# Kernel tuning notes

Hardware: AMD Instinct MI355X
Metric: run time of the kernel (lower is better)

Reference implementation:

```python
import jax, jax.numpy as jnp
import numpy as np

KH, KW = 3, 3
STRIDE, PAD = 2, 1
NEG_SLOPE = 0.2
EPS = 1e-5


def conv2d(x, w, stride, pad):
    return jax.lax.conv_general_dilated(
        x, w, window_strides=(stride, stride),
        padding=[(pad, pad), (pad, pad)],
        dimension_numbers=('NCHW', 'OIHW', 'NCHW'))


def deform_conv2d(x, offsets, w_def):
    # x: [B,C,H,W]; offsets: [B,2*K,Ho,Wo] (per-kernel-tap (dy,dx) pairs);
    # w_def: [Cout,Cin,KH,KW]. Matches torchvision DeformConv2d (v1, no mask).
    B, C, H, W = x.shape
    Ho, Wo = offsets.shape[2], offsets.shape[3]
    K = KH * KW
    off = offsets.reshape(B, K, 2, Ho, Wo)
    dy, dx = off[:, :, 0], off[:, :, 1]            # [B,K,Ho,Wo]

    ky = jnp.arange(KH).repeat(KW).astype(x.dtype)   # [K]
    kx = jnp.tile(jnp.arange(KW), KH).astype(x.dtype)
    base_y = (jnp.arange(Ho) * STRIDE - PAD).astype(x.dtype)  # [Ho]
    base_x = (jnp.arange(Wo) * STRIDE - PAD).astype(x.dtype)

    # sampling positions [B,K,Ho,Wo]
    py = base_y[None, None, :, None] + ky[None, :, None, None] + dy
    px = base_x[None, None, None, :] + kx[None, :, None, None] + dx

    y0f = jnp.floor(py); x0f = jnp.floor(px)
    wy1 = py - y0f; wy0 = 1.0 - wy1
    wx1 = px - x0f; wx0 = 1.0 - wx1
    y0 = y0f.astype(jnp.int32); x0 = x0f.astype(jnp.int32)
    y1 = y0 + 1; x1 = x0 + 1

    xt = jnp.transpose(x, (0, 2, 3, 1))  # [B,H,W,C] for channel-last gather
    bidx = jnp.arange(B)[:, None, None, None]

    def corner(yi, xi):
        valid = ((yi >= 0) & (yi < H) & (xi >= 0) & (xi < W)).astype(x.dtype)
        yc = jnp.clip(yi, 0, H - 1); xc = jnp.clip(xi, 0, W - 1)
        v = xt[bidx, yc, xc]                         # [B,K,Ho,Wo,C]
        return v * valid[..., None]

    sampled = (corner(y0, x0) * (wy0 * wx0)[..., None]
               + corner(y0, x1) * (wy0 * wx1)[..., None]
               + corner(y1, x0) * (wy1 * wx0)[..., None]
               + corner(y1, x1) * (wy1 * wx1)[..., None])  # [B,K,Ho,Wo,C]

    wk = w_def.reshape(w_def.shape[0], w_def.shape[1], K)   # [Cout,Cin,K]
    return jnp.einsum('bkhwc,ock->bohw', sampled, wk)


def leaky_relu(x):
    return jnp.where(x >= 0, x, NEG_SLOPE * x)


def instance_norm(x):
    mean = jnp.mean(x, axis=(2, 3), keepdims=True)
    var = jnp.var(x, axis=(2, 3), keepdims=True)
    return (x - mean) * jax.lax.rsqrt(var + EPS)


def setup_inputs() -> dict:
    key = jax.random.key(0)
    k1, k2, k3, k4 = jax.random.split(key, 4)
    B, Cin, H, W = 8, 256, 128, 128
    Cout = 256
    x = jax.random.normal(k1, (B, Cin, H, W), dtype=jnp.float32)
    # conv_offset weight: predicts 2*K offset channels
    w_off = jax.random.normal(k2, (2 * KH * KW, Cin, KH, KW), dtype=jnp.float32) * 0.01
    w_def = jax.random.normal(k3, (Cout, Cin, KH, KW), dtype=jnp.float32) * 0.02
    w_1x1 = jax.random.normal(k4, (Cout, Cout, 1, 1), dtype=jnp.float32) * 0.02
    return {"x": x, "w_off": w_off, "w_def": w_def, "w_1x1": w_1x1}


def reference(x, w_off, w_def, w_1x1):
    offsets = conv2d(x, w_off, STRIDE, PAD)          # [B,18,Ho,Wo]
    y = deform_conv2d(x, offsets, w_def)             # [B,Cout,Ho,Wo]
    y = leaky_relu(y)
    y = conv2d(y, w_1x1, 1, 0)
    y = instance_norm(y)
    return leaky_relu(y)
```

## Files before the change

kernel.cpp:

```cpp
#include <hip/hip_runtime.h>

#define B_   8
#define CIN  256
#define H_   128
#define W_   128
#define HO   64
#define WO   64
#define CO_  256
#define NEG  0.2f

typedef __attribute__((ext_vector_type(8))) _Float16 h16x8;
typedef __attribute__((ext_vector_type(4))) float f32x4;
typedef unsigned short u16;

#define OFF_OFS   0
#define WDEF_OFS  589824
#define W1_OFS    884736
#define WBOFF_OFS 917504
#define Y1_OFS    954368
#define XBF_OFS   5148672
#define TAP_OFS   21925888
#define WS_NEED_TAP ((21925888ull + 1179648ull) * 4ull)

__device__ __forceinline__ float lrelu(float v) { return v >= 0.f ? v : NEG * v; }

__device__ __forceinline__ u16 f2h(float f) {
    _Float16 h = (_Float16)f;
    return *(u16*)&h;
}

__device__ __forceinline__ void gld16(const void* g, void* l) {
    __builtin_amdgcn_global_load_lds((const __attribute__((address_space(1))) unsigned*)g,
                                     (__attribute__((address_space(3))) unsigned*)l, 16, 0, 0);
}

__global__ __launch_bounds__(256) void prep(
    const float* __restrict__ wdef, const float* __restrict__ w1,
    const float* __restrict__ woff,
    u16* __restrict__ wdefh, u16* __restrict__ w1h, u16* __restrict__ wboff)
{
    int i = blockIdx.x * 256 + threadIdx.x;
    if (i < 9 * 256 * 256) {
        int c  = i & 255;
        int co = (i >> 8) & 255;
        int k  = i >> 16;
        wdefh[i] = f2h(wdef[((size_t)co * 256 + c) * 9 + k]);
    }
    if (i < 65536) w1h[i] = f2h(w1[i]);
    if (i < 73728) {
        int j  = i & 7;
        int s  = (i >> 3) & 7;
        int co = (i >> 6) & 31;
        int ch = (i >> 11) & 3;
        int k  = i >> 13;
        int c  = ch * 64 + ((s ^ ((co >> 1) & 7)) << 3) + j;
        wboff[i] = (co < 18) ? f2h(woff[((size_t)co * 256 + c) * 9 + k]) : (u16)0;
    }
}

__global__ __launch_bounds__(256) void nchw2nhwc(
    const float* __restrict__ x, u16* __restrict__ xh)
{
    __shared__ float tile[64][128];
    int bid = blockIdx.x;
    int g = bid & 3;
    int y = (bid >> 2) & 127;
    int b = bid >> 9;
    int t = threadIdx.x;

    const float* src = x + ((size_t)(b * 256 + g * 64) * 128 + y) * 128;
#pragma unroll
    for (int p = 0; p < 8; ++p) {
        int i = p * 256 + t;
        int cc = i >> 5, x4 = (i & 31) * 4;
        *(float4*)&tile[cc][x4] = *(const float4*)(src + (size_t)cc * 16384 + x4);
    }
    __syncthreads();

    int xpos = t >> 1, h = t & 1;
    u16 buf[32];
#pragma unroll
    for (int j = 0; j < 32; ++j) buf[j] = f2h(tile[h * 32 + j][xpos]);
    u16* dst = xh + (((size_t)b * 128 + y) * 128 + xpos) * 256 + g * 64 + h * 32;
#pragma unroll
    for (int q = 0; q < 4; ++q)
        *(int4*)(dst + q * 8) = *(int4*)(buf + q * 8);
}

__global__ __launch_bounds__(256) void offconv_mfma(
    const u16* __restrict__ xh, const u16* __restrict__ wboff,
    float* __restrict__ off)
{
    __shared__ __align__(16) char smem[57728];
    u16* xrowU = (u16*)smem;
    u16* bU    = (u16*)(smem + 49536);

    int blk = blockIdx.x;
    blk = (blk & 7) * 64 + (blk >> 3);
    int b = blk >> 6, ho = blk & 63;
    int t = threadIdx.x;
    int lane = t & 63, w = t >> 6;
    int r = lane & 15, kg = lane >> 4;

    const u16* xB = xh + (size_t)b * (128 * 128 * 256);

    f32x4 acc[2];
    acc[0] = f32x4{0.f, 0.f, 0.f, 0.f};
    acc[1] = f32x4{0.f, 0.f, 0.f, 0.f};

    if (t < 24) {
        int ry = t >> 3, s = t & 7;
        *(int4*)(smem + (ry * 129 * 8 + s) * 16) = int4{0, 0, 0, 0};
    }

    for (int ch = 0; ch < 4; ++ch) {
        __syncthreads();
        for (int ry = 0; ry < 3; ++ry) {
            int y = 2 * ho - 1 + ry;
            int rowbase = (ry * 129 + 1) * 128;
            if ((unsigned)y < 128u) {
#pragma unroll
                for (int p = 0; p < 4; ++p) {
                    int u = p * 256 + t;
                    int xpi = u >> 3, s = u & 7;
                    int c8 = s ^ (((xpi + 1) >> 1) & 7);
                    gld16(xB + ((size_t)(y * 128 + xpi)) * 256 + ch * 64 + c8 * 8,
                          smem + rowbase + p * 4096 + w * 1024);
                }
            } else if (ch == 0) {
#pragma unroll
                for (int p = 0; p < 4; ++p)
                    *(int4*)(smem + rowbase + (p * 256 + t) * 16) = int4{0, 0, 0, 0};
            }
        }
        gld16(wboff + (size_t)(0 * 4 + ch) * 2048 + t * 8,
              smem + 49536 + w * 1024);
        __syncthreads();

        for (int k = 0; k < 9; ++k) {
            int buf = k & 1;
            if (k < 8)
                gld16(wboff + (size_t)((k + 1) * 4 + ch) * 2048 + t * 8,
                      smem + 49536 + (buf ^ 1) * 4096 + w * 1024);
            int ky = k / 3, kx = k - 3 * ky;
            int pixA = w * 16 + r;
            int xp = 2 * pixA + kx;
            int abase = (ky * 129 + xp) * 64;
            int swA = (xp >> 1) & 7;
#pragma unroll
            for (int ksub = 0; ksub < 2; ++ksub) {
                int lc = ksub * 4 + kg;
                h16x8 a = *(h16x8*)(xrowU + abase + ((lc ^ swA) << 3));
#pragma unroll
                for (int n = 0; n < 2; ++n) {
                    int co = n * 16 + r;
                    h16x8 bb = *(h16x8*)(bU + buf * 2048 + co * 64 +
                                         ((lc ^ ((co >> 1) & 7)) << 3));
                    acc[n] = __builtin_amdgcn_mfma_f32_16x16x32_f16(a, bb, acc[n], 0, 0, 0);
                }
            }
            __syncthreads();
        }
    }

#pragma unroll
    for (int n = 0; n < 2; ++n) {
        int co = n * 16 + r;
        if (co < 18) {
#pragma unroll
            for (int j = 0; j < 4; ++j) {
                int wo = w * 16 + kg * 4 + j;
                off[(((size_t)b * 18 + co) * 64 + ho) * 64 + wo] = acc[n][j];
            }
        }
    }
}

__global__ __launch_bounds__(256) void tapgen(
    const float* __restrict__ off, int4* __restrict__ tap)
{
    int bid = blockIdx.x;
    int b = bid >> 6, ho = bid & 63;
    for (int i = threadIdx.x; i < 576; i += 256) {
        int pix = i / 9, k = i - 9 * (i / 9);
        int ky = k / 3, kx = k - 3 * ky;
        float dy = off[(((size_t)b * 18 + 2 * k    ) * 64 + ho) * 64 + pix];
        float dx = off[(((size_t)b * 18 + 2 * k + 1) * 64 + ho) * 64 + pix];
        float py = (float)(ho * 2 - 1 + ky) + dy;
        float px = (float)(pix * 2 - 1 + kx) + dx;
        float y0f = floorf(py), x0f = floorf(px);
        int y0 = (int)y0f, x0i = (int)x0f;
        float wy1 = py - y0f, wx1 = px - x0f;
        float wy0 = 1.f - wy1, wx0 = 1.f - wx1;
        int y1i = y0 + 1, x1i = x0i + 1;
        bool vy0 = (unsigned)y0  < 128u;
        bool vy1 = (unsigned)y1i < 128u;
        bool vx0 = (unsigned)x0i < 128u;
        bool vx1 = (unsigned)x1i < 128u;
        int yc0 = min(max(y0, 0), 127), yc1 = min(max(y1i, 0), 127);
        int xc0 = min(max(x0i, 0), 127), xc1 = min(max(x1i, 0), 127);
        int4 e;
        e.x = (yc0 * 128 + xc0) * 512 | (xc1 - xc0) | ((yc1 - yc0) << 1);
        e.y = (int)((unsigned)f2h((vy0 && vx0) ? wy0 * wx0 : 0.f) |
                    ((unsigned)f2h((vy0 && vx1) ? wy0 * wx1 : 0.f) << 16));
        e.z = (int)((unsigned)f2h((vy1 && vx0) ? wy1 * wx0 : 0.f) |
                    ((unsigned)f2h((vy1 && vx1) ? wy1 * wx1 : 0.f) << 16));
        e.w = 0;
        tap[(size_t)bid * 576 + i] = e;
    }
}

__global__ __launch_bounds__(512, 4) void deform_tap(
    const u16* __restrict__ xh, const int4* __restrict__ tap,
    const u16* __restrict__ wdefh, u16* __restrict__ y1p)
{
    extern __shared__ __align__(16) char smem[];

    int blk = blockIdx.x;
    blk = (blk & 7) * 64 + (blk >> 3);
    int b = blk >> 6, ho = blk & 63;
    int t = threadIdx.x;
    int lane = t & 63, w = t >> 6;
    int r = lane & 15, kg = lane >> 4;
    int pixS = w * 8 + (lane >> 3);
    int cs   = lane & 7;

    f32x4 acc[4][2];
    f32x4 zz = {0.f, 0.f, 0.f, 0.f};
#pragma unroll
    for (int m = 0; m < 4; ++m)
#pragma unroll
        for (int n = 0; n < 2; ++n) acc[m][n] = zz;

    const int4* tapB = tap + (size_t)(b * 64 + ho) * 576 + pixS * 9;
    const char* xb2  = (const char*)(xh + (size_t)b * (128 * 128 * 256)) + cs * 16;

    int sbw = pixS * 128 + ((cs ^ (pixS & 7)) << 4);

    auto stage = [&](int k, int ch, int dbuf) {
        const u16* wk = wdefh + ((size_t)k << 16);
#pragma unroll
        for (int p2 = 0; p2 < 4; ++p2) {
            int i = p2 * 512 + t;
            int co = i >> 3, s = i & 7;
            gld16(wk + (size_t)co * 256 + ch * 64 + ((s ^ (co & 7)) << 3),
                  smem + dbuf * 32768 + p2 * 8192 + w * 1024);
        }
    };

    {
        stage(0, 0, 0);
        int4 e = tapB[0];
        int o00 = e.x & 0x7FFFFE00;
        int dxo = (e.x & 1) << 9;
        int dyo = (e.x & 2) << 15;
        h16x8 c00 = *(const h16x8*)(xb2 + o00);
        h16x8 c01 = *(const h16x8*)(xb2 + o00 + dxo);
        h16x8 c10 = *(const h16x8*)(xb2 + o00 + dyo);
        h16x8 c11 = *(const h16x8*)(xb2 + o00 + dyo + dxo);
        union U { int u; _Float16 h[2]; };
        U u01, u23;
        u01.u = e.y; u23.u = e.z;
        h16x8 v = c00 * u01.h[0] + c01 * u01.h[1] + c10 * u23.h[0] + c11 * u23.h[1];
        *(h16x8*)(smem + 65536 + sbw) = v;
    }
    __syncthreads();

    for (int p = 0; p < 36; ++p) {
        int cur = p & 1;
        bool nx = p < 35;
        int4 e;
        h16x8 c00, c01, c10, c11;
        if (nx) {
            int pn = p + 1;
            int chn = pn / 9, kn = pn - 9 * chn;
            e = tapB[kn];
            int o00 = e.x & 0x7FFFFE00;
            int dxo = (e.x & 1) << 9;
            int dyo = (e.x & 2) << 15;
            const char* base = xb2 + chn * 128;
            c00 = *(const h16x8*)(base + o00);
            c01 = *(const h16x8*)(base + o00 + dxo);
            c10 = *(const h16x8*)(base + o00 + dyo);
            c11 = *(const h16x8*)(base + o00 + dyo + dxo);
            stage(kn, chn, cur ^ 1);
        }
        {
            u16* wb = (u16*)(smem + cur * 32768);
            u16* sb = (u16*)(smem + 65536 + cur * 8192);
            h16x8 af[4], bfr[2];
            __builtin_amdgcn_s_setprio(1);
#pragma unroll
            for (int ksub = 0; ksub < 2; ++ksub) {
                int so = ((ksub * 4 + kg) ^ (r & 7)) << 3;
#pragma unroll
                for (int m = 0; m < 4; ++m)
                    af[m] = *(h16x8*)(sb + (m * 16 + r) * 64 + so);
#pragma unroll
                for (int n = 0; n < 2; ++n)
                    bfr[n] = *(h16x8*)(wb + (w * 32 + n * 16 + r) * 64 + so);
#pragma unroll
                for (int m = 0; m < 4; ++m)
#pragma unroll
                    for (int n = 0; n < 2; ++n)
                        acc[m][n] = __builtin_amdgcn_mfma_f32_16x16x32_f16(af[m], bfr[n], acc[m][n], 0, 0, 0);
            }
            __builtin_amdgcn_s_setprio(0);
        }
        if (nx) {
            union U { int u; _Float16 h[2]; };
            U u01, u23;
            u01.u = e.y; u23.u = e.z;
            h16x8 v = c00 * u01.h[0] + c01 * u01.h[1] + c10 * u23.h[0] + c11 * u23.h[1];
            *(h16x8*)(smem + 65536 + (cur ^ 1) * 8192 + sbw) = v;
        }
        __syncthreads();
    }

    u16* outT = (u16*)smem;
    int rg = lane >> 4;
#pragma unroll
    for (int m = 0; m < 4; ++m)
#pragma unroll
        for (int n = 0; n < 2; ++n) {
            int co = w * 32 + n * 16 + r;
#pragma unroll
            for (int j = 0; j < 4; ++j) {
                int prow = m * 16 + rg * 4 + j;
                outT[prow * 256 + co] = f2h(lrelu(acc[m][n][j]));
            }
        }
    __syncthreads();
    u16* dst = y1p + (size_t)(b * 64 + ho) * 16384;
#pragma unroll
    for (int p = 0; p < 4; ++p)
        *(int4*)((char*)dst + p * 8192 + t * 16) = *(int4*)(smem + p * 8192 + t * 16);
}

__global__ __launch_bounds__(512, 4) void deform_inline(
    const u16* __restrict__ xh, const float* __restrict__ off,
    const u16* __restrict__ wdefh, u16* __restrict__ y1p)
{
    extern __shared__ __align__(16) char smem[];

    int blk = blockIdx.x;
    blk = (blk & 7) * 64 + (blk >> 3);
    int b = blk >> 6, ho = blk & 63;
    int t = threadIdx.x;
    int lane = t & 63, w = t >> 6;
    int r = lane & 15, kg = lane >> 4;
    int pixS = w * 8 + (lane >> 3);
    int cs   = lane & 7;

    f32x4 acc[4][2];
    f32x4 zz = {0.f, 0.f, 0.f, 0.f};
#pragma unroll
    for (int m = 0; m < 4; ++m)
#pragma unroll
        for (int n = 0; n < 2; ++n) acc[m][n] = zz;

    const u16* xB = xh + (size_t)b * (128 * 128 * 256);

    int o00, o01, o10, o11;
    float f00, f01, f10, f11;

    auto coords = [&](int k) {
        int ky = k / 3, kx = k - 3 * ky;
        float dy = off[(((size_t)b * 18 + 2 * k    ) * 64 + ho) * 64 + pixS];
        float dx = off[(((size_t)b * 18 + 2 * k + 1) * 64 + ho) * 64 + pixS];
        float py = (float)(ho * 2 - 1 + ky) + dy;
        float px = (float)(pixS * 2 - 1 + kx) + dx;
        float y0f = floorf(py), x0f = floorf(px);
        int y0 = (int)y0f, x0i = (int)x0f;
        float wy1 = py - y0f, wx1 = px - x0f;
        float wy0 = 1.f - wy1, wx0 = 1.f - wx1;
        int y1i = y0 + 1, x1i = x0i + 1;
        bool vy0 = (unsigned)y0  < 128u;
        bool vy1 = (unsigned)y1i < 128u;
        bool vx0 = (unsigned)x0i < 128u;
        bool vx1 = (unsigned)x1i < 128u;
        int yc0 = min(max(y0, 0), 127), yc1 = min(max(y1i, 0), 127);
        int xc0 = min(max(x0i, 0), 127), xc1 = min(max(x1i, 0), 127);
        o00 = yc0 * 128 + xc0;  o01 = yc0 * 128 + xc1;
        o10 = yc1 * 128 + xc0;  o11 = yc1 * 128 + xc1;
        f00 = (vy0 && vx0) ? wy0 * wx0 : 0.f;
        f01 = (vy0 && vx1) ? wy0 * wx1 : 0.f;
        f10 = (vy1 && vx0) ? wy1 * wx0 : 0.f;
        f11 = (vy1 && vx1) ? wy1 * wx1 : 0.f;
    };

    auto stage = [&](int k, int ch, int dbuf) {
        const u16* wk = wdefh + ((size_t)k << 16);
#pragma unroll
        for (int p2 = 0; p2 < 4; ++p2) {
            int i = p2 * 512 + t;
            int co = i >> 3, s = i & 7;
            gld16(wk + (size_t)co * 256 + ch * 64 + ((s ^ (co & 7)) << 3),
                  smem + dbuf * 32768 + p2 * 8192 + w * 1024);
        }
    };

    auto sample = [&](int ch, int dbuf) {
        int cw = ch * 64 + cs * 8;
        const u16* q00 = xB + (size_t)o00 * 256 + cw;
        const u16* q01 = xB + (size_t)o01 * 256 + cw;
        const u16* q10 = xB + (size_t)o10 * 256 + cw;
        const u16* q11 = xB + (size_t)o11 * 256 + cw;
        h16x8 c00 = *(const h16x8*)q00;
        h16x8 c01 = *(const h16x8*)q01;
        h16x8 c10 = *(const h16x8*)q10;
        h16x8 c11 = *(const h16x8*)q11;
        _Float16 hf00 = (_Float16)f00, hf01 = (_Float16)f01;
        _Float16 hf10 = (_Float16)f10, hf11 = (_Float16)f11;
        h16x8 v = c00 * hf00 + c01 * hf01 + c10 * hf10 + c11 * hf11;
        *(h16x8*)(smem + 65536 + dbuf * 8192 + pixS * 128 + ((cs ^ (pixS & 7)) << 4)) = v;
    };

    coords(0);
    stage(0, 0, 0);
    sample(0, 0);
    __syncthreads();

    for (int p = 0; p < 36; ++p) {
        int cur = p & 1;
        if (p < 35) {
            int pn = p + 1;
            int chn = pn / 9, kn = pn - 9 * chn;
            stage(kn, chn, cur ^ 1);
            coords(kn);
            sample(chn, cur ^ 1);
        }
        u16* wb = (u16*)(smem + cur * 32768);
        u16* sb = (u16*)(smem + 65536 + cur * 8192);
        h16x8 af[4], bfr[2];
        __builtin_amdgcn_s_setprio(1);
#pragma unroll
        for (int ksub = 0; ksub < 2; ++ksub) {
            int so = ((ksub * 4 + kg) ^ (r & 7)) << 3;
#pragma unroll
            for (int m = 0; m < 4; ++m)
                af[m] = *(h16x8*)(sb + (m * 16 + r) * 64 + so);
#pragma unroll
            for (int n = 0; n < 2; ++n)
                bfr[n] = *(h16x8*)(wb + (w * 32 + n * 16 + r) * 64 + so);
#pragma unroll
            for (int m = 0; m < 4; ++m)
#pragma unroll
                for (int n = 0; n < 2; ++n)
                    acc[m][n] = __builtin_amdgcn_mfma_f32_16x16x32_f16(af[m], bfr[n], acc[m][n], 0, 0, 0);
        }
        __builtin_amdgcn_s_setprio(0);
        __syncthreads();
    }

    u16* outT = (u16*)smem;
    int rg = lane >> 4;
#pragma unroll
    for (int m = 0; m < 4; ++m)
#pragma unroll
        for (int n = 0; n < 2; ++n) {
            int co = w * 32 + n * 16 + r;
#pragma unroll
            for (int j = 0; j < 4; ++j) {
                int prow = m * 16 + rg * 4 + j;
                outT[prow * 256 + co] = f2h(lrelu(acc[m][n][j]));
            }
        }
    __syncthreads();
    u16* dst = y1p + (size_t)(b * 64 + ho) * 16384;
#pragma unroll
    for (int p = 0; p < 4; ++p)
        *(int4*)((char*)dst + p * 8192 + t * 16) = *(int4*)(smem + p * 8192 + t * 16);
}

__global__ __launch_bounds__(256) void conv1x1_mfma(
    const u16* __restrict__ y1p, const u16* __restrict__ w1h,
    float* __restrict__ out)
{
    __shared__ __align__(16) char smem[20480];
    u16* btile = (u16*)smem;
    u16* atile = (u16*)(smem + 16384);

    int blk = blockIdx.x;
    blk = (blk & 7) * 64 + (blk >> 3);
    int b = blk >> 6, ho = blk & 63;
    int t = threadIdx.x, lane = t & 63, w = t >> 6;
    int r = lane & 15, kg = lane >> 4;
    int sR = (r >> 1) & 3;

    f32x4 acc[4][4];
    f32x4 zz = {0.f, 0.f, 0.f, 0.f};
#pragma unroll
    for (int m = 0; m < 4; ++m)
#pragma unroll
        for (int n = 0; n < 4; ++n) acc[m][n] = zz;

    const u16* abase = y1p + (size_t)(b * 64 + ho) * 16384;

    for (int ch = 0; ch < 8; ++ch) {
#pragma unroll
        for (int p = 0; p < 4; ++p) {
            int slot = p * 256 + t;
            int o = slot >> 2, qq = slot & 3;
            gld16(w1h + o * 256 + ch * 32 + ((qq ^ ((o >> 1) & 3)) << 3),
                  smem + p * 4096 + (t >> 6) * 1024);
        }
        {
            int pix = t >> 2, qq = t & 3;
            gld16(abase + pix * 256 + ch * 32 + ((qq ^ ((pix >> 1) & 3)) << 3),
                  smem + 16384 + (t >> 6) * 1024);
        }
        __syncthreads();
        h16x8 af[4], bfr[4];
#pragma unroll
        for (int m = 0; m < 4; ++m)
            af[m] = *(h16x8*)(atile + (m * 16 + r) * 32 + ((kg ^ sR) << 3));
#pragma unroll
        for (int n = 0; n < 4; ++n)
            bfr[n] = *(h16x8*)(btile + (w * 64 + n * 16 + r) * 32 + ((kg ^ sR) << 3));
#pragma unroll
        for (int m = 0; m < 4; ++m)
#pragma unroll
            for (int n = 0; n < 4; ++n)
                acc[m][n] = __builtin_amdgcn_mfma_f32_16x16x32_f16(af[m], bfr[n], acc[m][n], 0, 0, 0);
        __syncthreads();
    }

    int rg = lane >> 4;
#pragma unroll
    for (int m = 0; m < 4; ++m)
#pragma unroll
        for (int n = 0; n < 4; ++n) {
            int o = w * 64 + n * 16 + r;
            int pix0 = m * 16 + rg * 4;
            float4 v;
            v.x = acc[m][n][0]; v.y = acc[m][n][1];
            v.z = acc[m][n][2]; v.w = acc[m][n][3];
            *(float4*)(out + ((size_t)(b * 256 + o) * 64 + ho) * 64 + pix0) = v;
        }
}

__global__ __launch_bounds__(256) void instnorm(float* __restrict__ out)
{
    int bc = blockIdx.x;
    float* p = out + (size_t)bc * 4096;
    int t = threadIdx.x;

    float4 v[4];
    float s1 = 0.f, s2 = 0.f;
#pragma unroll
    for (int i = 0; i < 4; ++i) {
        v[i] = *(const float4*)&p[(t + i * 256) * 4];
        s1 += v[i].x + v[i].y + v[i].z + v[i].w;
        s2 += v[i].x * v[i].x + v[i].y * v[i].y + v[i].z * v[i].z + v[i].w * v[i].w;
    }
#pragma unroll
    for (int o = 32; o > 0; o >>= 1) {
        s1 += __shfl_down(s1, o);
        s2 += __shfl_down(s2, o);
    }
    __shared__ float rs[8];
    __shared__ float mb[2];
    int wave = t >> 6;
    if ((t & 63) == 0) { rs[wave] = s1; rs[4 + wave] = s2; }
    __syncthreads();
    if (t == 0) {
        float a = rs[0] + rs[1] + rs[2] + rs[3];
        float qq = rs[4] + rs[5] + rs[6] + rs[7];
        float mean = a * (1.f / 4096.f);
        float var  = qq * (1.f / 4096.f) - mean * mean;
        mb[0] = mean;
        mb[1] = rsqrtf(var + 1e-5f);
    }
    __syncthreads();
    float mean = mb[0], inv = mb[1];
#pragma unroll
    for (int i = 0; i < 4; ++i) {
        float4 u = v[i];
        u.x = lrelu((u.x - mean) * inv);
        u.y = lrelu((u.y - mean) * inv);
        u.z = lrelu((u.z - mean) * inv);
        u.w = lrelu((u.w - mean) * inv);
        *(float4*)&p[(t + i * 256) * 4] = u;
    }
}

extern "C" void kernel_launch(void* const* d_in, const int* in_sizes, int n_in,
                              void* d_out, int out_size, void* d_ws, size_t ws_size,
                              hipStream_t stream)
{
    const float* x     = (const float*)d_in[0];
    const float* w_off = (const float*)d_in[1];
    const float* w_def = (const float*)d_in[2];
    const float* w1    = (const float*)d_in[3];
    float* out = (float*)d_out;
    float* ws  = (float*)d_ws;

    float* off   = ws + OFF_OFS;
    u16*   wdefh = (u16*)(ws + WDEF_OFS);
    u16*   w1h   = (u16*)(ws + W1_OFS);
    u16*   wboff = (u16*)(ws + WBOFF_OFS);
    u16*   y1p   = (u16*)(ws + Y1_OFS);
    u16*   xh    = (u16*)(ws + XBF_OFS);
    int4*  tap   = (int4*)(ws + TAP_OFS);

    const bool use_tap = ws_size >= WS_NEED_TAP;

    hipFuncSetAttribute((const void*)deform_tap,
                        hipFuncAttributeMaxDynamicSharedMemorySize, 81920);
    hipFuncSetAttribute((const void*)deform_inline,
                        hipFuncAttributeMaxDynamicSharedMemorySize, 81920);

    hipLaunchKernelGGL(prep,         dim3(2304), dim3(256), 0, stream, w_def, w1, w_off, wdefh, w1h, wboff);
    hipLaunchKernelGGL(nchw2nhwc,    dim3(4096), dim3(256), 0, stream, x, xh);
    hipLaunchKernelGGL(offconv_mfma, dim3(512),  dim3(256), 0, stream, xh, wboff, off);
    if (use_tap) {
        hipLaunchKernelGGL(tapgen,     dim3(512), dim3(256), 0, stream, off, tap);
        hipLaunchKernelGGL(deform_tap, dim3(512), dim3(512), 81920, stream, xh, tap, wdefh, y1p);
    } else {
        hipLaunchKernelGGL(deform_inline, dim3(512), dim3(512), 81920, stream, xh, off, wdefh, y1p);
    }
    hipLaunchKernelGGL(conv1x1_mfma, dim3(512),  dim3(256), 0, stream, y1p, w1h, out);
    hipLaunchKernelGGL(instnorm,     dim3(2048), dim3(256), 0, stream, out);
}
```

Measured before the change: 151.9 us.

## Fuse 1x1 conv into deformable conv kernel epilogue

The deformable-conv tile result (leaky-relu'd, fp16) is kept in swizzled shared memory and immediately multiplied by the 1x1 weight matrix with MFMA, with the weights double-buffered through LDS. Output is then written directly as fp32 to the final tensor. This removes the y1 intermediate write/read and a separate conv1x1 kernel launch. In exchange, the deform kernel gets a longer tail with extra synchronisation, register pressure, and every block re-streams the full 1x1 weight matrix.

```diff
diff --git a/kernel.cpp b/kernel.cpp
--- a/kernel.cpp
+++ b/kernel.cpp
@@ -210,9 +210,10 @@
     }
 }
 
-__global__ __launch_bounds__(512, 4) void deform_tap(
+__global__ __launch_bounds__(512, 4) void deform_fused(
     const u16* __restrict__ xh, const int4* __restrict__ tap,
-    const u16* __restrict__ wdefh, u16* __restrict__ y1p)
+    const u16* __restrict__ wdefh, const u16* __restrict__ w1h,
+    float* __restrict__ out)
 {
     extern __shared__ __align__(16) char smem[];
 
@@ -317,7 +318,7 @@
         __syncthreads();
     }
 
-    u16* outT = (u16*)smem;
+    char* outT = smem + 32768;
     int rg = lane >> 4;
 #pragma unroll
     for (int m = 0; m < 4; ++m)
@@ -327,14 +328,64 @@
 #pragma unroll
             for (int j = 0; j < 4; ++j) {
                 int prow = m * 16 + rg * 4 + j;
-                outT[prow * 256 + co] = f2h(lrelu(acc[m][n][j]));
+                *(u16*)(outT + prow * 512 + ((co * 2) ^ ((prow & 7) << 4))) =
+                    f2h(lrelu(acc[m][n][j]));
             }
         }
+
+    auto stage1 = [&](int k2, int dbuf) {
+#pragma unroll
+        for (int p2 = 0; p2 < 2; ++p2) {
+            int i = p2 * 512 + t;
+            int o = i >> 2, s = i & 3;
+            gld16(w1h + (size_t)o * 256 + k2 * 32 + ((s ^ (o & 3)) << 3),
+                  smem + dbuf * 16384 + p2 * 8192 + w * 1024);
+        }
+    };
+
+    stage1(0, 0);
+#pragma unroll
+    for (int m = 0; m < 4; ++m)
+#pragma unroll
+        for (int n = 0; n < 2; ++n) acc[m][n] = zz;
     __syncthreads();
-    u16* dst = y1p + (size_t)(b * 64 + ho) * 16384;
-#pragma unroll
-    for (int p = 0; p < 4; ++p)
-        *(int4*)((char*)dst + p * 8192 + t * 16) = *(int4*)(smem + p * 8192 + t * 16);
+
+    for (int k2 = 0; k2 < 8; ++k2) {
+        int cur = k2 & 1;
+        if (k2 < 7) stage1(k2 + 1, cur ^ 1);
+        h16x8 af[4], bfr[2];
+        __builtin_amdgcn_s_setprio(1);
+#pragma unroll
+        for (int m = 0; m < 4; ++m) {
+            int prow = m * 16 + r;
+            af[m] = *(h16x8*)(outT + prow * 512 +
+                              ((((k2 << 2) + kg) << 4) ^ ((prow & 7) << 4)));
+        }
+#pragma unroll
+        for (int n = 0; n < 2; ++n) {
+            int o = w * 32 + n * 16 + r;
+            bfr[n] = *(h16x8*)(smem + cur * 16384 + o * 64 + ((kg ^ (o & 3)) << 4));
+        }
+#pragma unroll
+        for (int m = 0; m < 4; ++m)
+#pragma unroll
+            for (int n = 0; n < 2; ++n)
+                acc[m][n] = __builtin_amdgcn_mfma_f32_16x16x32_f16(af[m], bfr[n], acc[m][n], 0, 0, 0);
+        __builtin_amdgcn_s_setprio(0);
+        __syncthreads();
+    }
+
+#pragma unroll
+    for (int m = 0; m < 4; ++m)
+#pragma unroll
+        for (int n = 0; n < 2; ++n) {
+            int o = w * 32 + n * 16 + r;
+            int pix0 = m * 16 + rg * 4;
+            float4 v;
+            v.x = acc[m][n][0]; v.y = acc[m][n][1];
+            v.z = acc[m][n][2]; v.w = acc[m][n][3];
+            *(float4*)(out + ((size_t)(b * 256 + o) * 64 + ho) * 64 + pix0) = v;
+        }
 }
 
 __global__ __launch_bounds__(512, 4) void deform_inline(
@@ -606,7 +657,7 @@
 
     const bool use_tap = ws_size >= WS_NEED_TAP;
 
-    hipFuncSetAttribute((const void*)deform_tap,
+    hipFuncSetAttribute((const void*)deform_fused,
                         hipFuncAttributeMaxDynamicSharedMemorySize, 81920);
     hipFuncSetAttribute((const void*)deform_inline,
                         hipFuncAttributeMaxDynamicSharedMemorySize, 81920);
@@ -615,11 +666,11 @@
     hipLaunchKernelGGL(nchw2nhwc,    dim3(4096), dim3(256), 0, stream, x, xh);
     hipLaunchKernelGGL(offconv_mfma, dim3(512),  dim3(256), 0, stream, xh, wboff, off);
     if (use_tap) {
-        hipLaunchKernelGGL(tapgen,     dim3(512), dim3(256), 0, stream, off, tap);
-        hipLaunchKernelGGL(deform_tap, dim3(512), dim3(512), 81920, stream, xh, tap, wdefh, y1p);
+        hipLaunchKernelGGL(tapgen,       dim3(512), dim3(256), 0, stream, off, tap);
+        hipLaunchKernelGGL(deform_fused, dim3(512), dim3(512), 81920, stream, xh, tap, wdefh, w1h, out);
     } else {
         hipLaunchKernelGGL(deform_inline, dim3(512), dim3(512), 81920, stream, xh, off, wdefh, y1p);
-    }
-    hipLaunchKernelGGL(conv1x1_mfma, dim3(512),  dim3(256), 0, stream, y1p, w1h, out);
+        hipLaunchKernelGGL(conv1x1_mfma,  dim3(512), dim3(256), 0, stream, y1p, w1h, out);
+    }
     hipLaunchKernelGGL(instnorm,     dim3(2048), dim3(256), 0, stream, out);
 }
```

Result: faster. 146.3 us (-3.7%).
